# Optimization experiments

Hardware: AMD Instinct MI355X
Metric: run time of the kernel (lower is better)

The kernel has to match this reference:

```python
import jax, jax.numpy as jnp
import numpy as np

N_ATOMS = 20000
N_CG = 1000
N_EDGES = 200000
FEAT = 128
N_RBF = 20
N_CONV = 3
CUTOFF = 5.0
EPS = 1e-15


def swish(x):
    return x * jax.nn.sigmoid(x)


def preprocess_r(r):
    # r: (n, 3) -> dist (n,), unit (n, 3)
    d = jnp.sqrt((r * r + EPS).sum(-1))
    return d, r / d[:, None]


def dist_embed(d, W, b):
    # PainnRadialBasis (learnable_k=False) + Dense + cosine envelope
    k = jnp.arange(1, N_RBF + 1, dtype=d.dtype)
    rbf = jnp.sin(k[None, :] * jnp.pi * d[:, None] / CUTOFF) / d[:, None]
    env = 0.5 * (jnp.cos(jnp.pi * d / CUTOFF) + 1.0) * (d < CUTOFF).astype(d.dtype)
    return (rbf @ W + b) * env[:, None]


def scatter_mean(x, idx, n):
    s = jax.ops.segment_sum(x, idx, num_segments=n)
    cnt = jax.ops.segment_sum(jnp.ones(idx.shape[0], x.dtype), idx, num_segments=n)
    cnt = jnp.maximum(cnt, 1.0)
    return s / cnt.reshape((n,) + (1,) * (x.ndim - 1))


def cg_encoder(z, xyz, cg_xyz, mapping, nbr_list, embed,
               msg_W1, msg_b1, msg_W2, msg_b2, msg_distW, msg_distb,
               upd_U, upd_V, upd_W1, upd_b1, upd_W2, upd_b2,
               cg_W1, cg_b1, cg_W2, cg_b2, cg_distW, cg_distb):
    s = embed[z]                                     # (N, F)
    v = jnp.zeros((s.shape[0], FEAT, 3), s.dtype)    # (N, F, 3)
    src, dst = nbr_list[:, 0], nbr_list[:, 1]
    r_ij = xyz[dst] - xyz[src]
    r_iI = xyz - cg_xyz[mapping]
    d_ij, u_ij = preprocess_r(r_ij)
    d_iI, u_iI = preprocess_r(r_iI)

    S_I = None
    V_I = None
    for i in range(N_CONV):
        # ---- MessageBlock ----
        phi = swish(s @ msg_W1[i] + msg_b1[i]) @ msg_W2[i] + msg_b2[i]          # (N, 3F)
        w_s = dist_embed(d_ij, msg_distW[i], msg_distb[i])                      # (E, 3F)
        inv = (phi[dst] * w_s).reshape(-1, 3, FEAT)                             # (E, 3, F)
        dv_ij = inv[:, 2, :, None] * u_ij[:, None, :] + inv[:, 0, :, None] * v[dst]
        s = s + jax.ops.segment_sum(inv[:, 1, :], src, num_segments=N_ATOMS)
        v = v + jax.ops.segment_sum(dv_ij, src, num_segments=N_ATOMS)
        # ---- UpdateBlock ----
        u_v = jnp.einsum('nfd,fg->ngd', v, upd_U[i])
        v_v = jnp.einsum('nfd,fg->ngd', v, upd_V[i])
        v_v_norm = jnp.sqrt((v_v * v_v + EPS).sum(-1))                          # (N, F)
        stack = swish(jnp.concatenate([s, v_v_norm], -1) @ upd_W1[i] + upd_b1[i]) @ upd_W2[i] + upd_b2[i]
        a_vv = stack[:, :FEAT, None]
        a_sv = stack[:, FEAT:2 * FEAT]
        a_ss = stack[:, 2 * FEAT:]
        v = v + u_v * a_vv
        s = s + (u_v * v_v).sum(-1) * a_sv + a_ss
        # ---- init CG features after first conv ----
        if i == 0:
            S_I = scatter_mean(s, mapping, N_CG)
            V_I = jnp.zeros((N_CG, FEAT, 3), s.dtype)
        # ---- ContractiveMessageBlock ----
        phi_cg = swish(s @ cg_W1[i] + cg_b1[i]) @ cg_W2[i] + cg_b2[i]           # (N, 3F)
        w_cg = dist_embed(d_iI, cg_distW[i], cg_distb[i])
        inv_cg = (phi_cg * w_cg).reshape(-1, 3, FEAT)
        dv_iI = inv_cg[:, 2, :, None] * u_iI[:, None, :] + inv_cg[:, 0, :, None] * v
        S_I = S_I + scatter_mean(inv_cg[:, 1, :], mapping, N_CG)
        V_I = V_I + scatter_mean(dv_iI, mapping, N_CG)
    return S_I


def setup_inputs() -> dict:
    key = jax.random.key(0)
    ks = jax.random.split(key, 20)
    p = lambda i, shape: jax.random.normal(ks[i], shape, jnp.float32) * 0.05
    return {
        'z': jax.random.randint(ks[0], (N_ATOMS,), 1, 100),
        'xyz': jax.random.normal(ks[1], (N_ATOMS, 3), jnp.float32),
        'cg_xyz': jax.random.normal(ks[2], (N_CG, 3), jnp.float32),
        'mapping': jax.random.randint(ks[3], (N_ATOMS,), 0, N_CG),
        'nbr_list': jax.random.randint(ks[4], (N_EDGES, 2), 0, N_ATOMS),
        'embed': p(5, (100, FEAT)).at[0].set(0.0),  # padding_idx=0
        'msg_W1': p(6, (N_CONV, FEAT, FEAT)), 'msg_b1': jnp.zeros((N_CONV, FEAT)),
        'msg_W2': p(7, (N_CONV, FEAT, 3 * FEAT)), 'msg_b2': jnp.zeros((N_CONV, 3 * FEAT)),
        'msg_distW': p(8, (N_CONV, N_RBF, 3 * FEAT)), 'msg_distb': jnp.zeros((N_CONV, 3 * FEAT)),
        'upd_U': p(9, (N_CONV, FEAT, FEAT)), 'upd_V': p(10, (N_CONV, FEAT, FEAT)),
        'upd_W1': p(11, (N_CONV, 2 * FEAT, FEAT)), 'upd_b1': jnp.zeros((N_CONV, FEAT)),
        'upd_W2': p(12, (N_CONV, FEAT, 3 * FEAT)), 'upd_b2': jnp.zeros((N_CONV, 3 * FEAT)),
        'cg_W1': p(13, (N_CONV, FEAT, FEAT)), 'cg_b1': jnp.zeros((N_CONV, FEAT)),
        'cg_W2': p(14, (N_CONV, FEAT, 3 * FEAT)), 'cg_b2': jnp.zeros((N_CONV, 3 * FEAT)),
        'cg_distW': p(15, (N_CONV, N_RBF, 3 * FEAT)), 'cg_distb': jnp.zeros((N_CONV, 3 * FEAT)),
    }


def reference(z, xyz, cg_xyz, mapping, nbr_list, embed,
              msg_W1, msg_b1, msg_W2, msg_b2, msg_distW, msg_distb,
              upd_U, upd_V, upd_W1, upd_b1, upd_W2, upd_b2,
              cg_W1, cg_b1, cg_W2, cg_b2, cg_distW, cg_distb):
    return cg_encoder(z, xyz, cg_xyz, mapping, nbr_list, embed,
                      msg_W1, msg_b1, msg_W2, msg_b2, msg_distW, msg_distb,
                      upd_U, upd_V, upd_W1, upd_b1, upd_W2, upd_b2,
                      cg_W1, cg_b1, cg_W2, cg_b2, cg_distW, cg_distb)
```

## Files before the change

kernel.cpp:

```cpp
#include <hip/hip_runtime.h>
#include <math.h>

#define N_ATOMS 20000
#define N_CG    1000
#define N_EDGES 200000
#define FEAT    128
#define NRBF    20
#define NCONV   3
#define CUTOFF  5.0f
#define PLANE   (N_ATOMS * FEAT)
#define PI_F    3.14159265358979323846f
#define LDH     130

#define PACK_PER_CONV 212992

typedef __attribute__((ext_vector_type(8))) short bf16x8;
typedef __attribute__((ext_vector_type(4))) float f32x4;

__device__ __forceinline__ void split2(float x, ushort& h, ushort& l)
{
    unsigned u  = __float_as_uint(x);
    unsigned hb = (u + 0x7FFFu + ((u >> 16) & 1u)) & 0xFFFF0000u;
    float    hf = __uint_as_float(hb);
    float    lf = x - hf;
    unsigned ul = __float_as_uint(lf);
    h = (ushort)(hb >> 16);
    l = (ushort)((ul + 0x7FFFu + ((ul >> 16) & 1u)) >> 16);
}

__device__ __forceinline__ float recon(const ushort* __restrict__ H,
                                       const ushort* __restrict__ L, size_t i)
{
    return __uint_as_float((unsigned)H[i] << 16) + __uint_as_float((unsigned)L[i] << 16);
}

__device__ __forceinline__ void splitv8(const float* hv, bf16x8& ah, bf16x8& al)
{
#pragma unroll
    for (int j = 0; j < 8; ++j) {
        ushort h, l;
        split2(hv[j], h, l);
        ah[j] = (short)h; al[j] = (short)l;
    }
}

#define MFMA3(ACC, AH_, AL_, BH_, BL_)                                              \
    ACC = __builtin_amdgcn_mfma_f32_16x16x32_bf16(AH_, BH_, ACC, 0, 0, 0);          \
    ACC = __builtin_amdgcn_mfma_f32_16x16x32_bf16(AH_, BL_, ACC, 0, 0, 0);          \
    ACC = __builtin_amdgcn_mfma_f32_16x16x32_bf16(AL_, BH_, ACC, 0, 0, 0);

template<int K1, int N2>
__global__ __launch_bounds__(256)
void mlp_fused(const ushort* __restrict__ AH, const ushort* __restrict__ AL,
               const ushort* __restrict__ B1h, const ushort* __restrict__ B1l,
               const float* __restrict__ b1,
               const ushort* __restrict__ B2h, const ushort* __restrict__ B2l,
               const float* __restrict__ b2, int bcol0,
               float* __restrict__ C)
{
    __shared__ float Hs[32 * LDH];
    const int tid  = threadIdx.x;
    const int lane = tid & 63;
    const int w    = tid >> 6;
    const int wm   = w & 1, wn = w >> 1;
    const int m0   = blockIdx.x * 32;
    const int l15  = lane & 15;
    const int koff = (lane >> 4) * 8;
    const int rowb = wm * 16;
    const int q4   = (lane >> 4) * 4;

    f32x4 acc1[4];
#pragma unroll
    for (int j = 0; j < 4; ++j) acc1[j] = (f32x4){0.f, 0.f, 0.f, 0.f};
    for (int k0 = 0; k0 < K1; k0 += 32) {
        size_t aa = (size_t)(m0 + rowb + l15) * K1 + k0 + koff;
        bf16x8 ah = *reinterpret_cast<const bf16x8*>(AH + aa);
        bf16x8 al = *reinterpret_cast<const bf16x8*>(AL + aa);
#pragma unroll
        for (int nf = 0; nf < 4; ++nf) {
            size_t ba = (size_t)(wn * 64 + nf * 16 + l15) * K1 + k0 + koff;
            bf16x8 bh = *reinterpret_cast<const bf16x8*>(B1h + ba);
            bf16x8 bl = *reinterpret_cast<const bf16x8*>(B1l + ba);
            MFMA3(acc1[nf], ah, al, bh, bl);
        }
    }
#pragma unroll
    for (int nf = 0; nf < 4; ++nf) {
        int col = wn * 64 + nf * 16 + l15;
        float bv = b1[col];
#pragma unroll
        for (int r = 0; r < 4; ++r) {
            float x = acc1[nf][r] + bv;
            x = x / (1.f + __expf(-x));
            Hs[(rowb + q4 + r) * LDH + col] = x;
        }
    }
    __syncthreads();

    constexpr int NF2  = N2 / 32;
    constexpr int WCOL = N2 / 2;
    f32x4 acc2[NF2];
#pragma unroll
    for (int j = 0; j < NF2; ++j) acc2[j] = (f32x4){0.f, 0.f, 0.f, 0.f};
    for (int k0 = 0; k0 < 128; k0 += 32) {
        const float* hp = &Hs[(rowb + l15) * LDH + k0 + koff];
        float hv[8];
#pragma unroll
        for (int j = 0; j < 4; ++j) hv[j] = hp[j];
#pragma unroll
        for (int j = 0; j < 4; ++j) hv[4 + j] = hp[4 + j];
        bf16x8 ah, al;
        splitv8(hv, ah, al);
#pragma unroll
        for (int nf = 0; nf < NF2; ++nf) {
            size_t ba = (size_t)(wn * WCOL + nf * 16 + l15) * 128 + k0 + koff;
            bf16x8 bh = *reinterpret_cast<const bf16x8*>(B2h + ba);
            bf16x8 bl = *reinterpret_cast<const bf16x8*>(B2l + ba);
            MFMA3(acc2[nf], ah, al, bh, bl);
        }
    }
#pragma unroll
    for (int nf = 0; nf < NF2; ++nf) {
        int col = wn * WCOL + nf * 16 + l15;
        float bv = b2 ? b2[bcol0 + col] : 0.f;
#pragma unroll
        for (int r = 0; r < 4; ++r) {
            int row = m0 + rowb + q4 + r;
            C[(size_t)row * N2 + col] = acc2[nf][r] + bv;
        }
    }
}

__global__ __launch_bounds__(256)
void k_update_mega(const ushort* __restrict__ vHp, const ushort* __restrict__ vLp,
                   const ushort* __restrict__ catH, const ushort* __restrict__ catL,
                   const ushort* __restrict__ BVh, const ushort* __restrict__ BVl,
                   const ushort* __restrict__ W1h, const ushort* __restrict__ W1l,
                   const float*  __restrict__ b1,
                   const ushort* __restrict__ W2h, const ushort* __restrict__ W2l,
                   const float*  __restrict__ b2,
                   const ushort* __restrict__ BUh, const ushort* __restrict__ BUl,
                   float* __restrict__ s,
                   ushort* __restrict__ sH, ushort* __restrict__ sL)
{
    __shared__ __align__(16) char smem[16640 + 49152];
    float*  Hs  = (float*)smem;
    float*  stk = (float*)(smem + 16640);
    ushort* nH  = (ushort*)(smem + 16640);
    ushort* nL  = (ushort*)(smem + 16640 + 8192);

    const int tid  = threadIdx.x;
    const int lane = tid & 63;
    const int w    = tid >> 6;
    const int wm   = w & 1, wn = w >> 1;
    const int m0   = blockIdx.x * 32;
    const int l15  = lane & 15;
    const int koff = (lane >> 4) * 8;
    const int rowb = wm * 16;
    const int q4   = (lane >> 4) * 4;

    f32x4 accV[3][4], accU[3][4];
#pragma unroll
    for (int d = 0; d < 3; ++d)
#pragma unroll
        for (int j = 0; j < 4; ++j) {
            accV[d][j] = (f32x4){0.f, 0.f, 0.f, 0.f};
            accU[d][j] = (f32x4){0.f, 0.f, 0.f, 0.f};
        }
    for (int k0 = 0; k0 < 128; k0 += 32) {
        bf16x8 ah[3], al[3];
#pragma unroll
        for (int d = 0; d < 3; ++d) {
            size_t aa = (size_t)d * PLANE + (size_t)(m0 + rowb + l15) * 128 + k0 + koff;
            ah[d] = *reinterpret_cast<const bf16x8*>(vHp + aa);
            al[d] = *reinterpret_cast<const bf16x8*>(vLp + aa);
        }
#pragma unroll
        for (int nf = 0; nf < 4; ++nf) {
            size_t ba = (size_t)(wn * 64 + nf * 16 + l15) * 128 + k0 + koff;
            bf16x8 bvh = *reinterpret_cast<const bf16x8*>(BVh + ba);
            bf16x8 bvl = *reinterpret_cast<const bf16x8*>(BVl + ba);
            bf16x8 buh = *reinterpret_cast<const bf16x8*>(BUh + ba);
            bf16x8 bul = *reinterpret_cast<const bf16x8*>(BUl + ba);
#pragma unroll
            for (int d = 0; d < 3; ++d) {
                MFMA3(accV[d][nf], ah[d], al[d], bvh, bvl);
            }
#pragma unroll
            for (int d = 0; d < 3; ++d) {
                MFMA3(accU[d][nf], ah[d], al[d], buh, bul);
            }
        }
    }
#pragma unroll
    for (int nf = 0; nf < 4; ++nf) {
        int col = wn * 64 + nf * 16 + l15;
#pragma unroll
        for (int r = 0; r < 4; ++r) {
            int lrow = rowb + q4 + r;
            float x = accV[0][nf][r], y = accV[1][nf][r], z = accV[2][nf][r];
            float nrm = sqrtf(x * x + y * y + z * z + 3e-15f);
            ushort h, l;
            split2(nrm, h, l);
            nH[lrow * 128 + col] = h;
            nL[lrow * 128 + col] = l;
        }
    }
    __syncthreads();

    f32x4 acc1[4];
#pragma unroll
    for (int j = 0; j < 4; ++j) acc1[j] = (f32x4){0.f, 0.f, 0.f, 0.f};
    for (int k0 = 0; k0 < 256; k0 += 32) {
        bf16x8 ah, al;
        if (k0 < 128) {
            size_t aa = (size_t)(m0 + rowb + l15) * 128 + k0 + koff;
            ah = *reinterpret_cast<const bf16x8*>(catH + aa);
            al = *reinterpret_cast<const bf16x8*>(catL + aa);
        } else {
            int la = (rowb + l15) * 128 + (k0 - 128) + koff;
            ah = *reinterpret_cast<const bf16x8*>(nH + la);
            al = *reinterpret_cast<const bf16x8*>(nL + la);
        }
#pragma unroll
        for (int nf = 0; nf < 4; ++nf) {
            size_t ba = (size_t)(wn * 64 + nf * 16 + l15) * 256 + k0 + koff;
            bf16x8 bh = *reinterpret_cast<const bf16x8*>(W1h + ba);
            bf16x8 bl = *reinterpret_cast<const bf16x8*>(W1l + ba);
            MFMA3(acc1[nf], ah, al, bh, bl);
        }
    }
#pragma unroll
    for (int nf = 0; nf < 4; ++nf) {
        int col = wn * 64 + nf * 16 + l15;
        float bv = b1[col];
#pragma unroll
        for (int r = 0; r < 4; ++r) {
            float x = acc1[nf][r] + bv;
            x = x / (1.f + __expf(-x));
            Hs[(rowb + q4 + r) * LDH + col] = x;
        }
    }
    __syncthreads();

    f32x4 acc2[12];
#pragma unroll
    for (int j = 0; j < 12; ++j) acc2[j] = (f32x4){0.f, 0.f, 0.f, 0.f};
    for (int k0 = 0; k0 < 128; k0 += 32) {
        const float* hp = &Hs[(rowb + l15) * LDH + k0 + koff];
        float hv[8];
#pragma unroll
        for (int j = 0; j < 8; ++j) hv[j] = hp[j];
        bf16x8 ah, al;
        splitv8(hv, ah, al);
#pragma unroll
        for (int nf = 0; nf < 12; ++nf) {
            size_t ba = (size_t)(wn * 192 + nf * 16 + l15) * 128 + k0 + koff;
            bf16x8 bh = *reinterpret_cast<const bf16x8*>(W2h + ba);
            bf16x8 bl = *reinterpret_cast<const bf16x8*>(W2l + ba);
            MFMA3(acc2[nf], ah, al, bh, bl);
        }
    }
#pragma unroll
    for (int nf = 0; nf < 12; ++nf) {
        int col = wn * 192 + nf * 16 + l15;
        float bv = b2[col];
#pragma unroll
        for (int r = 0; r < 4; ++r) {
            stk[(rowb + q4 + r) * 384 + col] = acc2[nf][r] + bv;
        }
    }
    __syncthreads();

    ushort* vHo = const_cast<ushort*>(vHp);
    ushort* vLo = const_cast<ushort*>(vLp);
#pragma unroll
    for (int nf = 0; nf < 4; ++nf) {
        int col = wn * 64 + nf * 16 + l15;
#pragma unroll
        for (int r = 0; r < 4; ++r) {
            int lrow = rowb + q4 + r;
            int row  = m0 + lrow;
            int idx  = row * FEAT + col;
            float avv = stk[lrow * 384 + col];
            float asv = stk[lrow * 384 + 128 + col];
            float ass = stk[lrow * 384 + 256 + col];
            float u0 = accU[0][nf][r], u1 = accU[1][nf][r], u2 = accU[2][nf][r];
            float w0 = accV[0][nf][r], w1 = accV[1][nf][r], w2 = accV[2][nf][r];
            float dot = u0 * w0 + u1 * w1 + u2 * w2;
            float n0 = recon(vHp, vLp, idx)                    + u0 * avv;
            float n1 = recon(vHp, vLp, (size_t)PLANE + idx)    + u1 * avv;
            float n2 = recon(vHp, vLp, (size_t)2 * PLANE + idx)+ u2 * avv;
            ushort h, l;
            split2(n0, h, l); vHo[idx] = h;             vLo[idx] = l;
            split2(n1, h, l); vHo[PLANE + idx] = h;     vLo[PLANE + idx] = l;
            split2(n2, h, l); vHo[2 * PLANE + idx] = h; vLo[2 * PLANE + idx] = l;
            float ns = s[idx] + dot * asv + ass;
            s[idx] = ns;
            split2(ns, h, l); sH[idx] = h; sL[idx] = l;
        }
    }
}

__global__ void k_pack_all(const float* __restrict__ msg_W1, const float* __restrict__ msg_W2,
                           const float* __restrict__ upd_V,  const float* __restrict__ upd_W1,
                           const float* __restrict__ upd_W2, const float* __restrict__ upd_U,
                           const float* __restrict__ cg_W1,  const float* __restrict__ cg_W2,
                           ushort* __restrict__ Bh, ushort* __restrict__ Bl)
{
    const int wid = blockIdx.y, conv = blockIdx.z;
    const float* W; int K, N, ldw, col0; size_t off;
    switch (wid) {
        case 0: W = msg_W1 + (size_t)conv * 16384; K = 128; N = 128; ldw = 128; col0 = 0;   off = 0;      break;
        case 1: W = msg_W2 + (size_t)conv * 49152; K = 128; N = 384; ldw = 384; col0 = 0;   off = 16384;  break;
        case 2: W = upd_V  + (size_t)conv * 16384; K = 128; N = 128; ldw = 128; col0 = 0;   off = 65536;  break;
        case 3: W = upd_W1 + (size_t)conv * 32768; K = 256; N = 128; ldw = 128; col0 = 0;   off = 81920;  break;
        case 4: W = upd_W2 + (size_t)conv * 49152; K = 128; N = 384; ldw = 384; col0 = 0;   off = 114688; break;
        case 5: W = upd_U  + (size_t)conv * 16384; K = 128; N = 128; ldw = 128; col0 = 0;   off = 163840; break;
        case 6: W = cg_W1  + (size_t)conv * 16384; K = 128; N = 128; ldw = 128; col0 = 0;   off = 180224; break;
        default:W = cg_W2  + (size_t)conv * 49152; K = 128; N = 128; ldw = 384; col0 = 128; off = 196608; break;
    }
    off += (size_t)conv * PACK_PER_CONV;
    int idx = blockIdx.x * 256 + threadIdx.x;
    if (idx >= K * N) return;
    int k = idx & (K - 1);
    int n = idx >> ((K == 256) ? 8 : 7);
    ushort h, l;
    split2(W[(size_t)k * ldw + col0 + n], h, l);
    Bh[off + (size_t)n * K + k] = h;
    Bl[off + (size_t)n * K + k] = l;
}

__global__ void k_s_init(const int* __restrict__ z, const float* __restrict__ embed,
                         float* __restrict__ s, ushort* __restrict__ sH, ushort* __restrict__ sL)
{
    int idx = blockIdx.x * blockDim.x + threadIdx.x;
    if (idx >= PLANE) return;
    int n = idx >> 7, g = idx & 127;
    float e = embed[z[n] * FEAT + g];
    s[idx] = e;
    ushort h, l;
    split2(e, h, l);
    sH[idx] = h; sL[idx] = l;
}

__global__ void k_atom_geo(const int* __restrict__ mapping,
                           const float* __restrict__ xyz, const float* __restrict__ cg_xyz,
                           float* __restrict__ rbf_a, float* __restrict__ env_a,
                           float* __restrict__ cnt)
{
    int n = blockIdx.x * blockDim.x + threadIdx.x;
    if (n >= N_ATOMS) return;
    int m = mapping[n];
    float dx = xyz[n * 3 + 0] - cg_xyz[m * 3 + 0];
    float dy = xyz[n * 3 + 1] - cg_xyz[m * 3 + 1];
    float dz = xyz[n * 3 + 2] - cg_xyz[m * 3 + 2];
    float d = sqrtf(dx * dx + dy * dy + dz * dz + 3e-15f);
    float env = (d < CUTOFF) ? 0.5f * (cosf(PI_F * d / CUTOFF) + 1.f) : 0.f;
    env_a[n] = env;
    float s = env / d;
#pragma unroll
    for (int k = 0; k < NRBF; ++k)
        rbf_a[n * NRBF + k] = sinf((k + 1) * PI_F * d / CUTOFF) * s;
    atomicAdd(&cnt[m], 1.f);
}

__global__ void k_deg(const int* __restrict__ nbr, int* __restrict__ deg)
{
    int e = blockIdx.x * blockDim.x + threadIdx.x;
    if (e < N_EDGES) atomicAdd(&deg[nbr[2 * e]], 1);
}

__global__ __launch_bounds__(1024)
void k_scan(const int* __restrict__ deg, int* __restrict__ rowptr)
{
    __shared__ int sh[1024];
    const int chunk = (N_ATOMS + 1023) / 1024;
    int t = threadIdx.x;
    int base = t * chunk;
    int sum = 0;
    for (int i = 0; i < chunk; ++i) {
        int idx = base + i;
        if (idx < N_ATOMS) sum += deg[idx];
    }
    sh[t] = sum;
    __syncthreads();
    for (int off = 1; off < 1024; off <<= 1) {
        int val = (t >= off) ? sh[t - off] : 0;
        __syncthreads();
        sh[t] += val;
        __syncthreads();
    }
    int run = (t == 0) ? 0 : sh[t - 1];
    for (int i = 0; i < chunk; ++i) {
        int idx = base + i;
        if (idx < N_ATOMS) { rowptr[idx] = run; run += deg[idx]; }
    }
}

__global__ void k_fill(const int* __restrict__ nbr, const float* __restrict__ xyz,
                       const int* __restrict__ rowptr, int* __restrict__ cursor,
                       int* __restrict__ rec_dst, float4* __restrict__ rec_u4,
                       float* __restrict__ rec_rbf)
{
    int e = blockIdx.x * blockDim.x + threadIdx.x;
    if (e >= N_EDGES) return;
    int src = nbr[2 * e], dst = nbr[2 * e + 1];
    int pos = atomicAdd(&cursor[src], 1);
    int q = rowptr[src] + pos;
    float dx = xyz[dst * 3 + 0] - xyz[src * 3 + 0];
    float dy = xyz[dst * 3 + 1] - xyz[src * 3 + 1];
    float dz = xyz[dst * 3 + 2] - xyz[src * 3 + 2];
    float d = sqrtf(dx * dx + dy * dy + dz * dz + 3e-15f);
    float env = (d < CUTOFF) ? 0.5f * (cosf(PI_F * d / CUTOFF) + 1.f) : 0.f;
    rec_dst[q] = dst;
    rec_u4[q] = make_float4(dx / d, dy / d, dz / d, env);
    float sc = env / d;
#pragma unroll
    for (int k = 0; k < NRBF; ++k)
        rec_rbf[(size_t)q * NRBF + k] = sinf((k + 1) * PI_F * d / CUTOFF) * sc;
}

#define EDGE_BLOCKS 2500
__global__ __launch_bounds__(512, 2)
void k_edge_seg(const int* __restrict__ rowptr, const int* __restrict__ deg,
                const int* __restrict__ rec_dst, const float4* __restrict__ rec_u4,
                const float* __restrict__ rec_rbf,
                const float* __restrict__ phi,
                const ushort* __restrict__ vHi, const ushort* __restrict__ vLi,
                ushort* __restrict__ vHo, ushort* __restrict__ vLo,
                float* __restrict__ s,
                ushort* __restrict__ catH, ushort* __restrict__ catL,
                const float* __restrict__ distW, const float* __restrict__ distb)
{
    const int tid    = threadIdx.x;
    const int slot   = tid >> 7;
    const int f      = tid & 127;
    const int slot_g = blockIdx.x * 4 + slot;
    const int nslots = EDGE_BLOCKS * 4;

    float wx[21], wy[21], wz[21];
#pragma unroll
    for (int k = 0; k < NRBF; ++k) {
        wx[k] = distW[k * 384 + f];
        wy[k] = distW[k * 384 + 128 + f];
        wz[k] = distW[k * 384 + 256 + f];
    }
    wx[20] = distb[f];
    wy[20] = distb[128 + f];
    wz[20] = distb[256 + f];
#pragma unroll
    for (int k = 0; k < 21; ++k) {
        asm volatile("" : "+v"(wx[k]), "+v"(wy[k]), "+v"(wz[k]));
    }

    for (int a = slot_g; a < N_ATOMS; a += nslots) {
        const int beg = rowptr[a];
        const int end = beg + deg[a];
        float s_acc = 0.f, vx = 0.f, vy = 0.f, vz = 0.f;

        for (int p = beg; p < end; p += 2) {
            const int  has2 = (p + 1 < end);
            const int  p1   = has2 ? p + 1 : p;
            const float m1  = has2 ? 1.f : 0.f;

            float4 u40 = rec_u4[p];
            float4 u41 = rec_u4[p1];
            int dst0 = rec_dst[p];
            int dst1 = rec_dst[p1];

            const float* ph0 = phi + (size_t)dst0 * 384 + f;
            const float* ph1 = phi + (size_t)dst1 * 384 + f;
            float p00 = ph0[0], p01 = ph0[128], p02 = ph0[256];
            float p10 = ph1[0], p11 = ph1[128], p12 = ph1[256];
            size_t di0 = (size_t)dst0 * FEAT + f;
            size_t di1 = (size_t)dst1 * FEAT + f;
            float v0x = recon(vHi, vLi, di0);
            float v0y = recon(vHi, vLi, PLANE + di0);
            float v0z = recon(vHi, vLi, 2 * (size_t)PLANE + di0);
            float v1x = recon(vHi, vLi, di1);
            float v1y = recon(vHi, vLi, PLANE + di1);
            float v1z = recon(vHi, vLi, 2 * (size_t)PLANE + di1);
            const float4* rb0 = reinterpret_cast<const float4*>(rec_rbf + (size_t)p  * NRBF);
            const float4* rb1 = reinterpret_cast<const float4*>(rec_rbf + (size_t)p1 * NRBF);
            float4 a0 = rb0[0], a1 = rb0[1], a2 = rb0[2], a3 = rb0[3], a4 = rb0[4];
            float4 b0 = rb1[0], b1 = rb1[1], b2 = rb1[2], b3 = rb1[3], b4 = rb1[4];

            const float rr0[21] = {a0.x, a0.y, a0.z, a0.w, a1.x, a1.y, a1.z, a1.w,
                                   a2.x, a2.y, a2.z, a2.w, a3.x, a3.y, a3.z, a3.w,
                                   a4.x, a4.y, a4.z, a4.w, u40.w};
            const float rr1[21] = {b0.x, b0.y, b0.z, b0.w, b1.x, b1.y, b1.z, b1.w,
                                   b2.x, b2.y, b2.z, b2.w, b3.x, b3.y, b3.z, b3.w,
                                   b4.x, b4.y, b4.z, b4.w, u41.w};
            float w00 = 0.f, w01 = 0.f, w02 = 0.f;
            float w10 = 0.f, w11 = 0.f, w12 = 0.f;
#pragma unroll
            for (int k = 0; k < 21; ++k) {
                w00 += rr0[k] * wx[k];
                w01 += rr0[k] * wy[k];
                w02 += rr0[k] * wz[k];
                w10 += rr1[k] * wx[k];
                w11 += rr1[k] * wy[k];
                w12 += rr1[k] * wz[k];
            }
            float i00 = p00 * w00, i01 = p01 * w01, i02 = p02 * w02;
            float i10 = (p10 * w10) * m1, i11 = (p11 * w11) * m1, i12 = (p12 * w12) * m1;
            vx += i02 * u40.x + i00 * v0x;
            vy += i02 * u40.y + i00 * v0y;
            vz += i02 * u40.z + i00 * v0z;
            s_acc += i01;
            vx += i12 * u41.x + i10 * v1x;
            vy += i12 * u41.y + i10 * v1y;
            vz += i12 * u41.z + i10 * v1z;
            s_acc += i11;
        }

        size_t si = (size_t)a * FEAT + f;
        float ns = s[si] + s_acc;
        s[si] = ns;
        float nx = recon(vHi, vLi, si)                    + vx;
        float ny = recon(vHi, vLi, PLANE + si)            + vy;
        float nz = recon(vHi, vLi, 2 * (size_t)PLANE + si)+ vz;
        ushort h, l;
        split2(nx, h, l); vHo[si] = h;             vLo[si] = l;
        split2(ny, h, l); vHo[PLANE + si] = h;     vLo[PLANE + si] = l;
        split2(nz, h, l); vHo[2 * PLANE + si] = h; vLo[2 * PLANE + si] = l;
        split2(ns, h, l);
        catH[(size_t)a * 128 + f] = h;
        catL[(size_t)a * 128 + f] = l;
    }
}

__global__ __launch_bounds__(128)
void k_cg_msg(const int* __restrict__ mapping, const float* __restrict__ phi_mid,
              const float* __restrict__ rbf_a, const float* __restrict__ env_a,
              const float* __restrict__ distW, const float* __restrict__ distb,
              const float* __restrict__ s_add, float* __restrict__ S_acc)
{
    int n = blockIdx.x;
    float env = env_a[n];
    int f = threadIdx.x;
    if (env == 0.f && s_add == nullptr) return;
    float val = s_add ? s_add[n * FEAT + f] : 0.f;
    if (env != 0.f) {
        __shared__ float sh_rbf[NRBF];
        if (f < NRBF) sh_rbf[f] = rbf_a[n * NRBF + f];
        __syncthreads();
        float w1 = 0.f;
#pragma unroll
        for (int k = 0; k < NRBF; ++k)
            w1 += sh_rbf[k] * distW[k * 384 + 128 + f];
        w1 += distb[128 + f] * env;
        val += phi_mid[n * FEAT + f] * w1;
    }
    atomicAdd(&S_acc[mapping[n] * FEAT + f], val);
}

__global__ void k_finalize(const float* __restrict__ S_acc, const float* __restrict__ cnt,
                           float* __restrict__ out, int add)
{
    int idx = blockIdx.x * blockDim.x + threadIdx.x;
    if (idx >= N_CG * FEAT) return;
    float val = S_acc[idx] / fmaxf(cnt[idx >> 7], 1.f);
    if (add) out[idx] += val;
    else     out[idx] = val;
}

extern "C" void kernel_launch(void* const* d_in, const int* in_sizes, int n_in,
                              void* d_out, int out_size, void* d_ws, size_t ws_size,
                              hipStream_t stream)
{
    const int*   z        = (const int*)d_in[0];
    const float* xyz      = (const float*)d_in[1];
    const float* cg_xyz   = (const float*)d_in[2];
    const int*   mapping  = (const int*)d_in[3];
    const int*   nbr      = (const int*)d_in[4];
    const float* embed    = (const float*)d_in[5];
    const float* msg_W1   = (const float*)d_in[6];
    const float* msg_b1   = (const float*)d_in[7];
    const float* msg_W2   = (const float*)d_in[8];
    const float* msg_b2   = (const float*)d_in[9];
    const float* msg_dW   = (const float*)d_in[10];
    const float* msg_db   = (const float*)d_in[11];
    const float* upd_U    = (const float*)d_in[12];
    const float* upd_V    = (const float*)d_in[13];
    const float* upd_W1   = (const float*)d_in[14];
    const float* upd_b1   = (const float*)d_in[15];
    const float* upd_W2   = (const float*)d_in[16];
    const float* upd_b2   = (const float*)d_in[17];
    const float* cg_W1    = (const float*)d_in[18];
    const float* cg_b1    = (const float*)d_in[19];
    const float* cg_W2    = (const float*)d_in[20];
    const float* cg_b2    = (const float*)d_in[21];
    const float* cg_dW    = (const float*)d_in[22];
    const float* cg_db    = (const float*)d_in[23];
    float* out = (float*)d_out;

    float* ws = (float*)d_ws;
    size_t o = 0;
    float* s      = ws + o; o += PLANE;
    float* uv     = ws + o; o += PLANE;
    float* phi    = ws + o; o += (size_t)N_ATOMS * 384;
    float* catpk  = ws + o; o += PLANE;
    float* spk    = ws + o; o += PLANE;
    float* vpkA   = ws + o; o += 3 * PLANE;
    float* vpkB   = ws + o; o += 3 * PLANE;
    float4* rec_u4 = (float4*)(ws + o); o += (size_t)N_EDGES * 4;
    float* rec_rbf = ws + o; o += (size_t)N_EDGES * NRBF;
    int*   rec_dst = (int*)(ws + o); o += N_EDGES;
    float* rbf_a  = ws + o; o += (size_t)N_ATOMS * NRBF;
    float* env_a  = ws + o; o += N_ATOMS;
    float* cnt    = ws + o; o += N_CG;
    float* S_acc  = ws + o; o += N_CG * FEAT;
    int*   deg    = (int*)(ws + o); o += N_ATOMS;
    int*   rowptr = (int*)(ws + o); o += N_ATOMS;
    int*   cursor = (int*)(ws + o); o += N_ATOMS;
    ushort* packH = (ushort*)(ws + o); o += (size_t)NCONV * PACK_PER_CONV / 2;
    ushort* packL = (ushort*)(ws + o); o += (size_t)NCONV * PACK_PER_CONV / 2;

    ushort* catH = (ushort*)catpk; ushort* catL = catH + (size_t)N_ATOMS * 128;
    ushort* sH = (ushort*)spk;  ushort* sL = sH + PLANE;
    ushort* vHa = (ushort*)vpkA; ushort* vLa = vHa + 3 * (size_t)PLANE;
    ushort* vHb = (ushort*)vpkB; ushort* vLb = vHb + 3 * (size_t)PLANE;

    hipMemsetAsync(vpkA, 0, sizeof(float) * 3 * PLANE, stream);
    hipMemsetAsync(cnt, 0, sizeof(float) * N_CG, stream);
    hipMemsetAsync(deg, 0, sizeof(int) * N_ATOMS, stream);
    hipMemsetAsync(cursor, 0, sizeof(int) * N_ATOMS, stream);
    k_pack_all<<<dim3(192, 8, 3), 256, 0, stream>>>(msg_W1, msg_W2, upd_V, upd_W1,
                                                    upd_W2, upd_U, cg_W1, cg_W2,
                                                    packH, packL);
    k_s_init<<<(PLANE + 255) / 256, 256, 0, stream>>>(z, embed, s, sH, sL);
    k_atom_geo<<<(N_ATOMS + 255) / 256, 256, 0, stream>>>(mapping, xyz, cg_xyz,
                                                          rbf_a, env_a, cnt);
    k_deg<<<(N_EDGES + 255) / 256, 256, 0, stream>>>(nbr, deg);
    k_scan<<<1, 1024, 0, stream>>>(deg, rowptr);
    k_fill<<<(N_EDGES + 255) / 256, 256, 0, stream>>>(nbr, xyz, rowptr, cursor,
                                                      rec_dst, rec_u4, rec_rbf);

    ushort* vHc = vHa; ushort* vLc = vLa;
    ushort* vHn = vHb; ushort* vLn = vLb;

    for (int i = 0; i < NCONV; ++i) {
        const float* mb1 = msg_b1 + (size_t)i * FEAT;
        const float* mb2 = msg_b2 + (size_t)i * 384;
        const float* mdW = msg_dW + (size_t)i * NRBF * 384;
        const float* mdb = msg_db + (size_t)i * 384;
        const float* ub1 = upd_b1 + (size_t)i * FEAT;
        const float* ub2 = upd_b2 + (size_t)i * 384;
        const float* cb1 = cg_b1  + (size_t)i * FEAT;
        const float* cb2 = cg_b2  + (size_t)i * 384;
        const float* cdW = cg_dW  + (size_t)i * NRBF * 384;
        const float* cdb = cg_db  + (size_t)i * 384;
        const size_t pb  = (size_t)i * PACK_PER_CONV;

        mlp_fused<128, 384><<<625, 256, 0, stream>>>(
            sH, sL, packH + pb + 0, packL + pb + 0, mb1,
            packH + pb + 16384, packL + pb + 16384, mb2, 0, phi);
        k_edge_seg<<<EDGE_BLOCKS, 512, 0, stream>>>(rowptr, deg, rec_dst, rec_u4,
                                                    rec_rbf, phi, vHc, vLc,
                                                    vHn, vLn, s, catH, catL,
                                                    mdW, mdb);

        k_update_mega<<<625, 256, 0, stream>>>(
            vHn, vLn, catH, catL,
            packH + pb + 65536,  packL + pb + 65536,
            packH + pb + 81920,  packL + pb + 81920,
            ub1,
            packH + pb + 114688, packL + pb + 114688,
            ub2,
            packH + pb + 163840, packL + pb + 163840,
            s, sH, sL);

        mlp_fused<128, 128><<<625, 256, 0, stream>>>(
            sH, sL, packH + pb + 180224, packL + pb + 180224, cb1,
            packH + pb + 196608, packL + pb + 196608, cb2, 128, uv);
        hipMemsetAsync(S_acc, 0, sizeof(float) * N_CG * FEAT, stream);
        k_cg_msg<<<N_ATOMS, 128, 0, stream>>>(mapping, uv, rbf_a, env_a, cdW, cdb,
                                              (i == 0) ? s : nullptr, S_acc);
        k_finalize<<<(N_CG * FEAT + 255) / 256, 256, 0, stream>>>(S_acc, cnt, out,
                                                                  i == 0 ? 0 : 1);

        ushort* th = vHn; ushort* tl = vLn;
        vHn = vHc; vLn = vLc;
        vHc = th;  vLc = tl;
    }
}
```

Before: 1.487 ms.

## Interleave v hi/lo bf16 halves into packed 32-bit words and drop stack smem

Stores the vector features as one packed 32-bit word per element (hi bf16 in the upper half, lo in the lower) instead of separate hi and lo planes. Gathers in the edge kernel then need one load per element instead of two scattered loads. The update kernel also keeps the second-MLP outputs in registers with a regrouped column mapping, removing the shared-memory stack and one barrier. In exchange, the MFMA A-operand loads in the update kernel become eight scalar 32-bit loads plus an unpack instead of vector bf16x8 loads.

After: 1.384 ms. -6.9%, faster.

```diff
diff --git a/kernel.cpp b/kernel.cpp
--- a/kernel.cpp
+++ b/kernel.cpp
@@ -28,10 +28,16 @@
     l = (ushort)((ul + 0x7FFFu + ((ul >> 16) & 1u)) >> 16);
 }
 
-__device__ __forceinline__ float recon(const ushort* __restrict__ H,
-                                       const ushort* __restrict__ L, size_t i)
-{
-    return __uint_as_float((unsigned)H[i] << 16) + __uint_as_float((unsigned)L[i] << 16);
+__device__ __forceinline__ float reconP(unsigned u)
+{
+    return __uint_as_float(u & 0xFFFF0000u) + __uint_as_float(u << 16);
+}
+
+__device__ __forceinline__ unsigned packP(float x)
+{
+    ushort h, l;
+    split2(x, h, l);
+    return ((unsigned)h << 16) | l;
 }
 
 __device__ __forceinline__ void splitv8(const float* hv, bf16x8& ah, bf16x8& al)
@@ -41,6 +47,17 @@
         ushort h, l;
         split2(hv[j], h, l);
         ah[j] = (short)h; al[j] = (short)l;
+    }
+}
+
+__device__ __forceinline__ void unpack8(const unsigned* __restrict__ p,
+                                        bf16x8& ah, bf16x8& al)
+{
+#pragma unroll
+    for (int j = 0; j < 8; ++j) {
+        unsigned u = p[j];
+        ah[j] = (short)(u >> 16);
+        al[j] = (short)(u & 0xFFFFu);
     }
 }
 
@@ -132,7 +149,7 @@
 }
 
 __global__ __launch_bounds__(256)
-void k_update_mega(const ushort* __restrict__ vHp, const ushort* __restrict__ vLp,
+void k_update_mega(unsigned* __restrict__ vP,
                    const ushort* __restrict__ catH, const ushort* __restrict__ catL,
                    const ushort* __restrict__ BVh, const ushort* __restrict__ BVl,
                    const ushort* __restrict__ W1h, const ushort* __restrict__ W1l,
@@ -143,11 +160,9 @@
                    float* __restrict__ s,
                    ushort* __restrict__ sH, ushort* __restrict__ sL)
 {
-    __shared__ __align__(16) char smem[16640 + 49152];
-    float*  Hs  = (float*)smem;
-    float*  stk = (float*)(smem + 16640);
-    ushort* nH  = (ushort*)(smem + 16640);
-    ushort* nL  = (ushort*)(smem + 16640 + 8192);
+    __shared__ float  Hs[32 * LDH];
+    __shared__ ushort nH[32 * 128];
+    __shared__ ushort nL[32 * 128];
 
     const int tid  = threadIdx.x;
     const int lane = tid & 63;
@@ -172,8 +187,10 @@
 #pragma unroll
         for (int d = 0; d < 3; ++d) {
             size_t aa = (size_t)d * PLANE + (size_t)(m0 + rowb + l15) * 128 + k0 + koff;
-            ah[d] = *reinterpret_cast<const bf16x8*>(vHp + aa);
-            al[d] = *reinterpret_cast<const bf16x8*>(vLp + aa);
+            unsigned u[8];
+#pragma unroll
+            for (int j = 0; j < 8; ++j) u[j] = vP[aa + j];
+            unpack8(u, ah[d], al[d]);
         }
 #pragma unroll
         for (int nf = 0; nf < 4; ++nf) {
@@ -254,49 +271,42 @@
         bf16x8 ah, al;
         splitv8(hv, ah, al);
 #pragma unroll
-        for (int nf = 0; nf < 12; ++nf) {
-            size_t ba = (size_t)(wn * 192 + nf * 16 + l15) * 128 + k0 + koff;
-            bf16x8 bh = *reinterpret_cast<const bf16x8*>(W2h + ba);
-            bf16x8 bl = *reinterpret_cast<const bf16x8*>(W2l + ba);
-            MFMA3(acc2[nf], ah, al, bh, bl);
-        }
-    }
-#pragma unroll
-    for (int nf = 0; nf < 12; ++nf) {
-        int col = wn * 192 + nf * 16 + l15;
-        float bv = b2[col];
-#pragma unroll
-        for (int r = 0; r < 4; ++r) {
-            stk[(rowb + q4 + r) * 384 + col] = acc2[nf][r] + bv;
-        }
-    }
-    __syncthreads();
-
-    ushort* vHo = const_cast<ushort*>(vHp);
-    ushort* vLo = const_cast<ushort*>(vLp);
+        for (int g = 0; g < 3; ++g) {
+#pragma unroll
+            for (int j = 0; j < 4; ++j) {
+                size_t ba = (size_t)(g * 128 + wn * 64 + j * 16 + l15) * 128 + k0 + koff;
+                bf16x8 bh = *reinterpret_cast<const bf16x8*>(W2h + ba);
+                bf16x8 bl = *reinterpret_cast<const bf16x8*>(W2l + ba);
+                MFMA3(acc2[g * 4 + j], ah, al, bh, bl);
+            }
+        }
+    }
+
 #pragma unroll
     for (int nf = 0; nf < 4; ++nf) {
         int col = wn * 64 + nf * 16 + l15;
+        float bavv = b2[col];
+        float basv = b2[128 + col];
+        float bass = b2[256 + col];
 #pragma unroll
         for (int r = 0; r < 4; ++r) {
-            int lrow = rowb + q4 + r;
-            int row  = m0 + lrow;
-            int idx  = row * FEAT + col;
-            float avv = stk[lrow * 384 + col];
-            float asv = stk[lrow * 384 + 128 + col];
-            float ass = stk[lrow * 384 + 256 + col];
+            int row = m0 + rowb + q4 + r;
+            size_t idx = (size_t)row * FEAT + col;
+            float avv = acc2[nf][r]     + bavv;
+            float asv = acc2[4 + nf][r] + basv;
+            float ass = acc2[8 + nf][r] + bass;
             float u0 = accU[0][nf][r], u1 = accU[1][nf][r], u2 = accU[2][nf][r];
             float w0 = accV[0][nf][r], w1 = accV[1][nf][r], w2 = accV[2][nf][r];
             float dot = u0 * w0 + u1 * w1 + u2 * w2;
-            float n0 = recon(vHp, vLp, idx)                    + u0 * avv;
-            float n1 = recon(vHp, vLp, (size_t)PLANE + idx)    + u1 * avv;
-            float n2 = recon(vHp, vLp, (size_t)2 * PLANE + idx)+ u2 * avv;
-            ushort h, l;
-            split2(n0, h, l); vHo[idx] = h;             vLo[idx] = l;
-            split2(n1, h, l); vHo[PLANE + idx] = h;     vLo[PLANE + idx] = l;
-            split2(n2, h, l); vHo[2 * PLANE + idx] = h; vLo[2 * PLANE + idx] = l;
+            float n0 = reconP(vP[idx])                      + u0 * avv;
+            float n1 = reconP(vP[PLANE + idx])              + u1 * avv;
+            float n2 = reconP(vP[2 * (size_t)PLANE + idx])  + u2 * avv;
+            vP[idx] = packP(n0);
+            vP[PLANE + idx] = packP(n1);
+            vP[2 * (size_t)PLANE + idx] = packP(n2);
             float ns = s[idx] + dot * asv + ass;
             s[idx] = ns;
+            ushort h, l;
             split2(ns, h, l); sH[idx] = h; sL[idx] = l;
         }
     }
@@ -427,8 +437,7 @@
                 const int* __restrict__ rec_dst, const float4* __restrict__ rec_u4,
                 const float* __restrict__ rec_rbf,
                 const float* __restrict__ phi,
-                const ushort* __restrict__ vHi, const ushort* __restrict__ vLi,
-                ushort* __restrict__ vHo, ushort* __restrict__ vLo,
+                const unsigned* __restrict__ vPi, unsigned* __restrict__ vPo,
                 float* __restrict__ s,
                 ushort* __restrict__ catH, ushort* __restrict__ catL,
                 const float* __restrict__ distW, const float* __restrict__ distb)
@@ -475,12 +484,12 @@
             float p10 = ph1[0], p11 = ph1[128], p12 = ph1[256];
             size_t di0 = (size_t)dst0 * FEAT + f;
             size_t di1 = (size_t)dst1 * FEAT + f;
-            float v0x = recon(vHi, vLi, di0);
-            float v0y = recon(vHi, vLi, PLANE + di0);
-            float v0z = recon(vHi, vLi, 2 * (size_t)PLANE + di0);
-            float v1x = recon(vHi, vLi, di1);
-            float v1y = recon(vHi, vLi, PLANE + di1);
-            float v1z = recon(vHi, vLi, 2 * (size_t)PLANE + di1);
+            float v0x = reconP(vPi[di0]);
+            float v0y = reconP(vPi[PLANE + di0]);
+            float v0z = reconP(vPi[2 * (size_t)PLANE + di0]);
+            float v1x = reconP(vPi[di1]);
+            float v1y = reconP(vPi[PLANE + di1]);
+            float v1z = reconP(vPi[2 * (size_t)PLANE + di1]);
             const float4* rb0 = reinterpret_cast<const float4*>(rec_rbf + (size_t)p  * NRBF);
             const float4* rb1 = reinterpret_cast<const float4*>(rec_rbf + (size_t)p1 * NRBF);
             float4 a0 = rb0[0], a1 = rb0[1], a2 = rb0[2], a3 = rb0[3], a4 = rb0[4];
@@ -518,13 +527,13 @@
         size_t si = (size_t)a * FEAT + f;
         float ns = s[si] + s_acc;
         s[si] = ns;
-        float nx = recon(vHi, vLi, si)                    + vx;
-        float ny = recon(vHi, vLi, PLANE + si)            + vy;
-        float nz = recon(vHi, vLi, 2 * (size_t)PLANE + si)+ vz;
+        float nx = reconP(vPi[si])                     + vx;
+        float ny = reconP(vPi[PLANE + si])             + vy;
+        float nz = reconP(vPi[2 * (size_t)PLANE + si]) + vz;
+        vPo[si] = packP(nx);
+        vPo[PLANE + si] = packP(ny);
+        vPo[2 * (size_t)PLANE + si] = packP(nz);
         ushort h, l;
-        split2(nx, h, l); vHo[si] = h;             vLo[si] = l;
-        split2(ny, h, l); vHo[PLANE + si] = h;     vLo[PLANE + si] = l;
-        split2(nz, h, l); vHo[2 * PLANE + si] = h; vLo[2 * PLANE + si] = l;
         split2(ns, h, l);
         catH[(size_t)a * 128 + f] = h;
         catL[(size_t)a * 128 + f] = l;
@@ -603,8 +612,8 @@
     float* phi    = ws + o; o += (size_t)N_ATOMS * 384;
     float* catpk  = ws + o; o += PLANE;
     float* spk    = ws + o; o += PLANE;
-    float* vpkA   = ws + o; o += 3 * PLANE;
-    float* vpkB   = ws + o; o += 3 * PLANE;
+    unsigned* vPA = (unsigned*)(ws + o); o += 3 * PLANE;
+    unsigned* vPB = (unsigned*)(ws + o); o += 3 * PLANE;
     float4* rec_u4 = (float4*)(ws + o); o += (size_t)N_EDGES * 4;
     float* rec_rbf = ws + o; o += (size_t)N_EDGES * NRBF;
     int*   rec_dst = (int*)(ws + o); o += N_EDGES;
@@ -620,10 +629,8 @@
 
     ushort* catH = (ushort*)catpk; ushort* catL = catH + (size_t)N_ATOMS * 128;
     ushort* sH = (ushort*)spk;  ushort* sL = sH + PLANE;
-    ushort* vHa = (ushort*)vpkA; ushort* vLa = vHa + 3 * (size_t)PLANE;
-    ushort* vHb = (ushort*)vpkB; ushort* vLb = vHb + 3 * (size_t)PLANE;
-
-    hipMemsetAsync(vpkA, 0, sizeof(float) * 3 * PLANE, stream);
+
+    hipMemsetAsync(vPA, 0, sizeof(unsigned) * 3 * PLANE, stream);
     hipMemsetAsync(cnt, 0, sizeof(float) * N_CG, stream);
     hipMemsetAsync(deg, 0, sizeof(int) * N_ATOMS, stream);
     hipMemsetAsync(cursor, 0, sizeof(int) * N_ATOMS, stream);
@@ -638,8 +645,8 @@
     k_fill<<<(N_EDGES + 255) / 256, 256, 0, stream>>>(nbr, xyz, rowptr, cursor,
                                                       rec_dst, rec_u4, rec_rbf);
 
-    ushort* vHc = vHa; ushort* vLc = vLa;
-    ushort* vHn = vHb; ushort* vLn = vLb;
+    unsigned* vPc = vPA;
+    unsigned* vPn = vPB;
 
     for (int i = 0; i < NCONV; ++i) {
         const float* mb1 = msg_b1 + (size_t)i * FEAT;
@@ -658,12 +665,11 @@
             sH, sL, packH + pb + 0, packL + pb + 0, mb1,
             packH + pb + 16384, packL + pb + 16384, mb2, 0, phi);
         k_edge_seg<<<EDGE_BLOCKS, 512, 0, stream>>>(rowptr, deg, rec_dst, rec_u4,
-                                                    rec_rbf, phi, vHc, vLc,
-                                                    vHn, vLn, s, catH, catL,
-                                                    mdW, mdb);
+                                                    rec_rbf, phi, vPc, vPn, s,
+                                                    catH, catL, mdW, mdb);
 
         k_update_mega<<<625, 256, 0, stream>>>(
-            vHn, vLn, catH, catL,
+            vPn, catH, catL,
             packH + pb + 65536,  packL + pb + 65536,
             packH + pb + 81920,  packL + pb + 81920,
             ub1,
@@ -681,8 +687,6 @@
         k_finalize<<<(N_CG * FEAT + 255) / 256, 256, 0, stream>>>(S_acc, cnt, out,
                                                                   i == 0 ? 0 : 1);
 
-        ushort* th = vHn; ushort* tl = vLn;
-        vHn = vHc; vLn = vLc;
-        vHc = th;  vLc = tl;
-    }
-}
+        unsigned* t = vPn; vPn = vPc; vPc = t;
+    }
+}
```
